# Performance work log

Hardware: AMD Instinct MI355X
Metric: run time of the kernel (lower is better)

## Reference

```python
import jax, jax.numpy as jnp
import numpy as np

B, S, D, H = 64, 256, 2048, 16
HD = D // H  # 128
MAXS = 256


def setup_inputs() -> dict:
    key = jax.random.key(0)
    ks = jax.random.split(key, 16)
    sc = 0.02
    inp = {
        "q": jax.random.normal(ks[0], (B, S, D), jnp.float32),
        "k": jax.random.normal(ks[1], (B, S, D), jnp.float32),
        "v": jax.random.normal(ks[2], (B, S, D), jnp.float32),
        "attention_mask": jax.random.randint(ks[3], (B, S), 0, 2, jnp.int32),
        # projection weights, torch Linear convention: y = x @ W.T + b
        "Wq": jax.random.normal(ks[4], (D, D), jnp.float32) * sc,
        "bq": jnp.zeros((D,), jnp.float32),
        "Wk": jax.random.normal(ks[5], (D, D), jnp.float32) * sc,
        "bk": jnp.zeros((D,), jnp.float32),
        "Wv": jax.random.normal(ks[6], (D, D), jnp.float32) * sc,
        "bv": jnp.zeros((D,), jnp.float32),
        "Wo": jax.random.normal(ks[7], (D, D), jnp.float32) * sc,
        "bo": jnp.zeros((D,), jnp.float32),
        # additive per-head bias table (max_sequence_length=256)
        "bias_table": jax.random.normal(ks[8], (H, MAXS, MAXS), jnp.float32) * 0.1,
    }
    return inp


def reference(q, k, v, attention_mask, Wq, bq, Wk, bk, Wv, bv, Wo, bo, bias_table):
    def proj(x, W, b):  # (B,S,D) -> (B,H,S,HD)
        y = x @ W.T + b
        return y.reshape(B, S, H, HD).transpose(0, 2, 1, 3)

    qh = proj(q, Wq, bq)
    kh = proj(k, Wk, bk)
    vh = proj(v, Wv, bv)

    # (B,H,Sq,Sk) scores
    scores = jnp.einsum("bhqd,bhkd->bhqk", qh, kh) / jnp.sqrt(jnp.float32(HD))
    scores = scores + bias_table[None, :, :S, :S]
    # mask: (B,Sk) -> (B,1,1,Sk); masked_fill where mask==0
    neg_inf = jnp.finfo(scores.dtype).min
    scores = jnp.where(attention_mask[:, None, None, :] == 0, neg_inf, scores)
    probs = jax.nn.softmax(scores, axis=-1)  # dropout p=0.0 -> identity
    out = jnp.einsum("bhqk,bhkd->bhqd", probs, vh)
    out = out.transpose(0, 2, 1, 3).reshape(B, S, D)
    return out @ Wo.T + bo
```

## Files before the change

### kernel.cpp

```cpp
#include <hip/hip_runtime.h>
#include <hip/hip_bf16.h>

typedef __attribute__((ext_vector_type(4))) float f32x4;
typedef __attribute__((ext_vector_type(8))) short s16x8;
typedef __attribute__((ext_vector_type(4))) unsigned short u16x4;
typedef __attribute__((ext_vector_type(8))) unsigned short u16x8;
typedef __attribute__((ext_vector_type(4))) int i32x4;

#define NB 64
#define NS 256
#define ND 2048
#define NH 16
#define NHD 128

__device__ __forceinline__ unsigned short f2bf(float f){
  unsigned int u = __float_as_uint(f);
  u += 0x7fffu + ((u >> 16) & 1u);
  return (unsigned short)(u >> 16);
}

__device__ __forceinline__ void gload16(const void* g, void* l){
  __builtin_amdgcn_global_load_lds(
    (const __attribute__((address_space(1))) unsigned int*)g,
    (__attribute__((address_space(3))) unsigned int*)l, 16, 0, 0);
}

#define SBAR()  __builtin_amdgcn_sched_barrier(0)
#define BARRIER() do{ SBAR(); __builtin_amdgcn_s_barrier(); SBAR(); }while(0)
#define WAIT_LGKM0() do{ asm volatile("s_waitcnt lgkmcnt(0)" ::: "memory"); SBAR(); }while(0)
#define WAIT_VM0()   do{ asm volatile("s_waitcnt vmcnt(0)"   ::: "memory"); SBAR(); }while(0)
#define WAIT_VM4()   do{ asm volatile("s_waitcnt vmcnt(4)"   ::: "memory"); SBAR(); }while(0)

__global__ __launch_bounds__(256) void wconv(const float* __restrict__ s,
                                             unsigned short* __restrict__ d, int n8){
  int i = blockIdx.x*256 + threadIdx.x;
  if (i >= n8) return;
  f32x4 a = *(const f32x4*)(s + (size_t)i*8);
  f32x4 b = *(const f32x4*)(s + (size_t)i*8 + 4);
  u16x8 u;
  #pragma unroll
  for (int r=0;r<4;r++){ u[r]=f2bf(a[r]); u[4+r]=f2bf(b[r]); }
  *(u16x8*)(d + (size_t)i*8) = u;
}

__global__ __launch_bounds__(256) void wconv4(
  const float* __restrict__ s0, const float* __restrict__ s1,
  const float* __restrict__ s2, const float* __restrict__ s3,
  unsigned short* __restrict__ d0, unsigned short* __restrict__ d1,
  unsigned short* __restrict__ d2, unsigned short* __restrict__ d3)
{
  int j = blockIdx.x >> 11;
  const float* s = (j==0)?s0:(j==1)?s1:(j==2)?s2:s3;
  unsigned short* d = (j==0)?d0:(j==1)?d1:(j==2)?d2:d3;
  int i = (blockIdx.x & 2047)*256 + threadIdx.x;
  f32x4 a = *(const f32x4*)(s + (size_t)i*8);
  f32x4 b = *(const f32x4*)(s + (size_t)i*8 + 4);
  u16x8 u;
  #pragma unroll
  for (int r=0;r<4;r++){ u[r]=f2bf(a[r]); u[4+r]=f2bf(b[r]); }
  *(u16x8*)(d + (size_t)i*8) = u;
}

#define GEMM_COMMON_DECLS \
  extern __shared__ __attribute__((aligned(16))) char ldsb[]; \
  const int tid  = threadIdx.x; \
  const int lane = tid & 63, wid = tid >> 6; \
  const int g = lane >> 4, l15 = lane & 15; \
  const int wm = wid >> 2, wn = wid & 3; \
  const int nwg = gridDim.x, bid = blockIdx.x; \
  const int swz = (bid & 7) * (nwg >> 3) + (bid >> 3); \
  const int mt = swz >> 3, nt = swz & 7; \
  const int m0 = mt*256, n0 = nt*256; \
  const int srow_l = tid >> 3, slot = tid & 7;

#define RD_A(buf, qa) do{ \
    _Pragma("unroll") for (int i_=0;i_<4;i_++){ \
      int hr = (qa)*64 + i_*16 + l15; \
      const char* p_ = ldsb + (buf)*65536 + wm*16384 + hr*128; \
      _Pragma("unroll") for (int ks_=0;ks_<2;ks_++) \
        av[i_][ks_] = *(const s16x8*)(p_ + (((ks_*4+g) ^ (hr&7))*16)); } }while(0)

#define RD_B(buf, dst, qb) do{ \
    _Pragma("unroll") for (int j_=0;j_<2;j_++){ \
      int hc = (wn&1)*64 + (qb)*32 + j_*16 + l15; \
      const char* p_ = ldsb + (buf)*65536 + 32768 + (wn>>1)*16384 + hc*128; \
      _Pragma("unroll") for (int ks_=0;ks_<2;ks_++) \
        dst[j_][ks_] = *(const s16x8*)(p_ + (((ks_*4+g) ^ (hc&7))*16)); } }while(0)

#define MFMA_PH(qa, qb, bv) do{ \
    __builtin_amdgcn_s_setprio(1); \
    _Pragma("unroll") for (int i_=0;i_<4;i_++) \
      _Pragma("unroll") for (int j_=0;j_<2;j_++) \
        _Pragma("unroll") for (int ks_=0;ks_<2;ks_++) \
          acc[(qa)*4+i_][(qb)*2+j_] = __builtin_amdgcn_mfma_f32_16x16x32_bf16( \
              av[i_][ks_], bv[j_][ks_], acc[(qa)*4+i_][(qb)*2+j_], 0,0,0); \
    __builtin_amdgcn_s_setprio(0); }while(0)

#define GEMM_EPILOGUE(OUTMODE_) \
  _Pragma("unroll") \
  for (int jx=0;jx<4;jx++){ \
    int n = n0 + wn*64 + ((jx>>1)<<5) + ((jx&1)<<4) + l15; \
    float bj = bias[n]; \
    _Pragma("unroll") \
    for (int i=0;i<8;i++){ \
      int mb = m0 + wm*128 + ((i>>2)<<6) + ((i&3)<<4) + g*4; \
      if ((OUTMODE_) == 2){ \
        float* O = (float*)Out; \
        _Pragma("unroll") for (int r=0;r<4;r++) O[(size_t)(mb+r)*ND + n] = acc[i][jx][r] + bj; \
      } else if ((OUTMODE_) == 0){ \
        unsigned short* O = (unsigned short*)Out; \
        int bb = mb >> 8, h = n >> 7, d = n & 127, s0 = mb & 255; \
        _Pragma("unroll") for (int r=0;r<4;r++) \
          O[(((size_t)bb*NH + h)*NS + s0 + r)*NHD + d] = f2bf(acc[i][jx][r] + bj); \
      } else { \
        unsigned short* O = (unsigned short*)Out; \
        int bb = mb >> 8, h = n >> 7, d = n & 127, s0 = mb & 255; \
        u16x4 u; \
        _Pragma("unroll") for (int r=0;r<4;r++) u[r] = f2bf(acc[i][jx][r] + bj); \
        *(u16x4*)(O + (((size_t)bb*NH + h)*NHD + d)*NS + s0) = u; \
      } \
    } \
  }

template<int OUTMODE>
__global__ __launch_bounds__(512, 2) void gemm256(
    const unsigned short* __restrict__ A, const unsigned short* __restrict__ Bw,
    const float* __restrict__ bias, void* __restrict__ Out)
{
  GEMM_COMMON_DECLS
  const int scol = ((slot ^ (srow_l & 7)) * 8);
  const unsigned short* gsrc[4];
  gsrc[0] = A  + (size_t)(m0 +       srow_l)*ND + scol;
  gsrc[1] = A  + (size_t)(m0 + 128 + srow_l)*ND + scol;
  gsrc[2] = Bw + (size_t)(n0 +       srow_l)*ND + scol;
  gsrc[3] = Bw + (size_t)(n0 + 128 + srow_l)*ND + scol;

#define STAGE(buf, p, kt) do{ \
    const unsigned short* s_ = gsrc[p] + (kt); \
    char* d_ = ldsb + (buf)*65536 + ((p)>>1)*32768 + ((p)&1)*16384 + tid*16; \
    gload16(s_, d_); gload16(s_ + (size_t)64*ND, d_ + 8192); }while(0)

#define HALF(d, ktA, ktB, wmode) do{ \
    RD_A(d,0); RD_B(d,bva,0); \
    if ((ktA)>=0) STAGE((d)^1, 0, ktA); \
    WAIT_LGKM0(); \
    MFMA_PH(0,0,bva); \
    BARRIER(); \
    RD_B(d,bvb,1); \
    if ((ktA)>=0) STAGE((d)^1, 1, ktA); \
    WAIT_LGKM0(); \
    MFMA_PH(0,1,bvb); \
    BARRIER(); \
    RD_A(d,1); \
    if ((ktB)>=0) STAGE(d, 2, ktB); \
    WAIT_LGKM0(); \
    MFMA_PH(1,0,bva); \
    BARRIER(); \
    if ((ktB)>=0) STAGE(d, 3, ktB); \
    MFMA_PH(1,1,bvb); \
    if ((wmode)==0){ WAIT_VM4(); } \
    else if ((wmode)==1){ WAIT_VM0(); } \
    BARRIER(); \
  }while(0)

  f32x4 acc[8][4];
  s16x8 av[4][2], bva[2][2], bvb[2][2];

  STAGE(0,0,0); STAGE(0,1,0); STAGE(0,2,0); STAGE(0,3,0);
  STAGE(1,2,64); STAGE(1,3,64);
  #pragma unroll
  for (int i=0;i<8;i++)
    #pragma unroll
    for (int j=0;j<4;j++) acc[i][j] = f32x4{0.f,0.f,0.f,0.f};
  WAIT_VM4();
  BARRIER();

  for (int t = 0; t < 15; ++t) {
    HALF(0, (2*t+1)*64, (2*t+2)*64, 0);
    HALF(1, (2*t+2)*64, (2*t+3)*64, 0);
  }
  HALF(0, 31*64, -1, 1);
  HALF(1, -1, -1, -1);

  GEMM_EPILOGUE(OUTMODE)
#undef STAGE
#undef HALF
}

__global__ __launch_bounds__(256, 2) void attn_fused5(
  const unsigned short* __restrict__ Qh, const unsigned short* __restrict__ Kh,
  const unsigned short* __restrict__ VT, const int* __restrict__ mask,
  const float* __restrict__ bias_table, unsigned short* __restrict__ AO)
{
  __shared__ unsigned short KV[256*128];
  char* KVb = (char*)KV;
  const int bid = blockIdx.x;
  const int bh = (((bid >> 3) >> 2) << 3) | (bid & 7);
  const int qt = (bid >> 3) & 3;
  const int b = bh >> 4, h = bh & 15;
  const int tid = threadIdx.x, lane = tid & 63, w = tid >> 6;
  const int g = lane >> 4, l15 = lane & 15;
  const int q = qt*64 + w*16 + l15;

  {
    const unsigned short* Ksrc = Kh + (size_t)bh*NS*NHD;
    int r0 = tid >> 4, sl = tid & 15;
    #pragma unroll
    for (int c=0;c<16;c++){
      int row = c*16 + r0;
      gload16(Ksrc + (size_t)row*NHD + ((sl ^ (row&7))*8), KVb + c*4096 + tid*16);
    }
  }
  const unsigned short* Qrow = Qh + ((size_t)bh*NS + q)*NHD;
  s16x8 bq[4];
  #pragma unroll
  for (int kk=0;kk<4;kk++) bq[kk] = *(const s16x8*)(Qrow + kk*32 + g*8);

  WAIT_VM0();
  BARRIER();

  f32x4 c[16];
  __builtin_amdgcn_s_setprio(1);
  #pragma unroll
  for (int kb=0;kb<16;kb++){
    c[kb] = f32x4{0.f,0.f,0.f,0.f};
    int row = kb*16 + l15;
    #pragma unroll
    for (int kk=0;kk<4;kk++){
      s16x8 a = *(const s16x8*)(KVb + row*256 + (((kk*4+g) ^ (row&7))*16));
      c[kb] = __builtin_amdgcn_mfma_f32_16x16x32_bf16(a, bq[kk], c[kb], 0,0,0);
    }
  }
  __builtin_amdgcn_s_setprio(0);

  WAIT_LGKM0();
  BARRIER();

  {
    const unsigned short* Vsrc = VT + (size_t)bh*NHD*NS;
    int r0 = tid >> 5, sl = tid & 31;
    #pragma unroll
    for (int c2=0;c2<16;c2++){
      int row = c2*8 + r0;
      gload16(Vsrc + (size_t)row*NS + ((sl ^ (row&7))*8), KVb + c2*4096 + tid*16);
    }
  }

  const float scale = 0.08838834764831845f;
  const float* brow = bias_table + ((size_t)h*NS + q)*NS;
  const int*   mrow = mask + b*NS;
  float mx = -3.0e38f;
  #pragma unroll
  for (int kb=0;kb<16;kb++){
    f32x4 b4 = *(const f32x4*)(brow + kb*16 + g*4);
    i32x4 m4 = *(const i32x4*)(mrow + kb*16 + g*4);
    #pragma unroll
    for (int r=0;r<4;r++){
      float val = (m4[r] != 0) ? (c[kb][r]*scale + b4[r]) : -3.0e38f;
      c[kb][r] = val;
      mx = fmaxf(mx, val);
    }
  }
  mx = fmaxf(mx, __shfl_xor(mx, 16));
  mx = fmaxf(mx, __shfl_xor(mx, 32));
  float sum = 0.f;
  #pragma unroll
  for (int kb=0;kb<16;kb++)
    #pragma unroll
    for (int r=0;r<4;r++){
      float pv = __expf(c[kb][r] - mx);
      c[kb][r] = pv; sum += pv;
    }
  sum += __shfl_xor(sum, 16);
  sum += __shfl_xor(sum, 32);
  float inv = 1.f / sum;

  unsigned int pk[16][2];
  #pragma unroll
  for (int kb=0;kb<16;kb++){
    pk[kb][0] = (unsigned int)f2bf(c[kb][0]*inv) | ((unsigned int)f2bf(c[kb][1]*inv) << 16);
    pk[kb][1] = (unsigned int)f2bf(c[kb][2]*inv) | ((unsigned int)f2bf(c[kb][3]*inv) << 16);
  }

  WAIT_VM0();
  BARRIER();

  const int s0l = l15 + ((g&1)<<5), s1l = s0l + 16;
  const int sel = g >> 1;
  s16x8 pb[8];
  #pragma unroll
  for (int kk=0;kk<8;kk++){
    unsigned int e0 = (unsigned int)__shfl((int)pk[2*kk][0],   s0l);
    unsigned int e1 = (unsigned int)__shfl((int)pk[2*kk][1],   s0l);
    unsigned int e2 = (unsigned int)__shfl((int)pk[2*kk][0],   s1l);
    unsigned int e3 = (unsigned int)__shfl((int)pk[2*kk][1],   s1l);
    unsigned int o0 = (unsigned int)__shfl((int)pk[2*kk+1][0], s0l);
    unsigned int o1 = (unsigned int)__shfl((int)pk[2*kk+1][1], s0l);
    unsigned int o2 = (unsigned int)__shfl((int)pk[2*kk+1][0], s1l);
    unsigned int o3 = (unsigned int)__shfl((int)pk[2*kk+1][1], s1l);
    union { unsigned int wd[4]; s16x8 v; } u_;
    u_.wd[0] = sel ? o0 : e0; u_.wd[1] = sel ? o1 : e1;
    u_.wd[2] = sel ? o2 : e2; u_.wd[3] = sel ? o3 : e3;
    pb[kk] = u_.v;
  }

  f32x4 oacc[8];
  __builtin_amdgcn_s_setprio(1);
  #pragma unroll
  for (int dt=0;dt<8;dt++){
    oacc[dt] = f32x4{0.f,0.f,0.f,0.f};
    int row = dt*16 + l15;
    #pragma unroll
    for (int kk=0;kk<8;kk++){
      s16x8 a = *(const s16x8*)(KVb + row*512 + (((kk*4+g) ^ (row&7))*16));
      oacc[dt] = __builtin_amdgcn_mfma_f32_16x16x32_bf16(a, pb[kk], oacc[dt], 0,0,0);
    }
  }
  __builtin_amdgcn_s_setprio(0);

  #pragma unroll
  for (int dt=0;dt<8;dt++){
    u16x4 u;
    #pragma unroll
    for (int r=0;r<4;r++) u[r] = f2bf(oacc[dt][r]);
    *(u16x4*)(AO + ((size_t)b*NS + q)*ND + h*NHD + dt*16 + g*4) = u;
  }
}

extern "C" void kernel_launch(void* const* d_in, const int* in_sizes, int n_in,
                              void* d_out, int out_size, void* d_ws, size_t ws_size,
                              hipStream_t stream)
{
  const float* q  = (const float*)d_in[0];
  const float* k  = (const float*)d_in[1];
  const float* v  = (const float*)d_in[2];
  const int* mask = (const int*)d_in[3];
  const float* Wq = (const float*)d_in[4];
  const float* bq = (const float*)d_in[5];
  const float* Wk = (const float*)d_in[6];
  const float* bk = (const float*)d_in[7];
  const float* Wv = (const float*)d_in[8];
  const float* bv = (const float*)d_in[9];
  const float* Wo = (const float*)d_in[10];
  const float* bo = (const float*)d_in[11];
  const float* bias_table = (const float*)d_in[12];

  char* ws = (char*)d_ws;
  unsigned short* Wqb = (unsigned short*)(ws + 0);
  unsigned short* Wkb = (unsigned short*)(ws + 8388608);
  unsigned short* Wvb = (unsigned short*)(ws + 16777216);
  unsigned short* Wob = (unsigned short*)(ws + 25165824);
  unsigned short* tmp = (unsigned short*)(ws + 33554432);
  unsigned short* Qh  = (unsigned short*)(ws + 100663296);
  unsigned short* Kh  = (unsigned short*)(ws + 167772160);
  unsigned short* VT  = (unsigned short*)(ws + 234881024);
  unsigned short* AO  = (unsigned short*)(ws + 301989888);

  hipFuncSetAttribute((const void*)gemm256<0>, hipFuncAttributeMaxDynamicSharedMemorySize, 131072);
  hipFuncSetAttribute((const void*)gemm256<1>, hipFuncAttributeMaxDynamicSharedMemorySize, 131072);
  hipFuncSetAttribute((const void*)gemm256<2>, hipFuncAttributeMaxDynamicSharedMemorySize, 131072);

  wconv4<<<8192,256,0,stream>>>(Wq,Wk,Wv,Wo, Wqb,Wkb,Wvb,Wob);

  const float* acts[3] = {q, k, v};
  const unsigned short* wgt[3] = {Wqb, Wkb, Wvb};
  const float* bia[3] = {bq, bk, bv};
  unsigned short* outs[3] = {Qh, Kh, VT};

  for (int x = 0; x < 3; ++x) {
    wconv<<<16384,256,0,stream>>>(acts[x], tmp, 4194304);
    if (x < 2)
      gemm256<0><<<512,512,131072,stream>>>(tmp, wgt[x], bia[x], outs[x]);
    else
      gemm256<1><<<512,512,131072,stream>>>(tmp, wgt[x], bia[x], outs[x]);
  }

  attn_fused5<<<4096,256,0,stream>>>(Qh,Kh,VT,mask,bias_table,AO);
  gemm256<2><<<512,512,131072,stream>>>(AO,Wob,bo,(float*)d_out);
}
```

Measured before the change: 724.5 us.

## Restage GEMM tiles two steps ahead, drop grid swizzle, prefetch attention bias/mask

The GEMM main loop now refills the buffer it has just finished reading with the tile two steps ahead, as B and then A halves, instead of splitting each tile's loads across both buffers. The vmcnt wait is adjusted to leave that batch of loads in flight. The block-to-tile swizzle is removed, so tiles map directly from the block index, which changes L2 reuse of A and W across concurrent blocks. The attention kernel issues bias-table and mask loads before the QK MFMA loop so their latency overlaps compute, at the cost of about 128 extra VGPRs per thread, which may hurt occupancy.

```diff
diff --git a/kernel.cpp b/kernel.cpp
--- a/kernel.cpp
+++ b/kernel.cpp
@@ -29,7 +29,7 @@
 #define BARRIER() do{ SBAR(); __builtin_amdgcn_s_barrier(); SBAR(); }while(0)
 #define WAIT_LGKM0() do{ asm volatile("s_waitcnt lgkmcnt(0)" ::: "memory"); SBAR(); }while(0)
 #define WAIT_VM0()   do{ asm volatile("s_waitcnt vmcnt(0)"   ::: "memory"); SBAR(); }while(0)
-#define WAIT_VM4()   do{ asm volatile("s_waitcnt vmcnt(4)"   ::: "memory"); SBAR(); }while(0)
+#define WAIT_VM8()   do{ asm volatile("s_waitcnt vmcnt(8)"   ::: "memory"); SBAR(); }while(0)
 
 __global__ __launch_bounds__(256) void wconv(const float* __restrict__ s,
                                              unsigned short* __restrict__ d, int n8){
@@ -67,9 +67,8 @@
   const int lane = tid & 63, wid = tid >> 6; \
   const int g = lane >> 4, l15 = lane & 15; \
   const int wm = wid >> 2, wn = wid & 3; \
-  const int nwg = gridDim.x, bid = blockIdx.x; \
-  const int swz = (bid & 7) * (nwg >> 3) + (bid >> 3); \
-  const int mt = swz >> 3, nt = swz & 7; \
+  const int bid = blockIdx.x; \
+  const int mt = bid >> 3, nt = bid & 7; \
   const int m0 = mt*256, n0 = nt*256; \
   const int srow_l = tid >> 3, slot = tid & 7;
 
@@ -140,25 +139,23 @@
     char* d_ = ldsb + (buf)*65536 + ((p)>>1)*32768 + ((p)&1)*16384 + tid*16; \
     gload16(s_, d_); gload16(s_ + (size_t)64*ND, d_ + 8192); }while(0)
 
-#define HALF(d, ktA, ktB, wmode) do{ \
+#define HALF(d, ktN, wmode) do{ \
     RD_A(d,0); RD_B(d,bva,0); \
-    if ((ktA)>=0) STAGE((d)^1, 0, ktA); \
     WAIT_LGKM0(); \
     MFMA_PH(0,0,bva); \
     BARRIER(); \
     RD_B(d,bvb,1); \
-    if ((ktA)>=0) STAGE((d)^1, 1, ktA); \
     WAIT_LGKM0(); \
     MFMA_PH(0,1,bvb); \
     BARRIER(); \
     RD_A(d,1); \
-    if ((ktB)>=0) STAGE(d, 2, ktB); \
+    if ((ktN)>=0){ STAGE(d,2,ktN); STAGE(d,3,ktN); } \
     WAIT_LGKM0(); \
     MFMA_PH(1,0,bva); \
     BARRIER(); \
-    if ((ktB)>=0) STAGE(d, 3, ktB); \
+    if ((ktN)>=0){ STAGE(d,0,ktN); STAGE(d,1,ktN); } \
     MFMA_PH(1,1,bvb); \
-    if ((wmode)==0){ WAIT_VM4(); } \
+    if ((wmode)==0){ WAIT_VM8(); } \
     else if ((wmode)==1){ WAIT_VM0(); } \
     BARRIER(); \
   }while(0)
@@ -167,27 +164,27 @@
   s16x8 av[4][2], bva[2][2], bvb[2][2];
 
   STAGE(0,0,0); STAGE(0,1,0); STAGE(0,2,0); STAGE(0,3,0);
-  STAGE(1,2,64); STAGE(1,3,64);
+  STAGE(1,0,64); STAGE(1,1,64); STAGE(1,2,64); STAGE(1,3,64);
   #pragma unroll
   for (int i=0;i<8;i++)
     #pragma unroll
     for (int j=0;j<4;j++) acc[i][j] = f32x4{0.f,0.f,0.f,0.f};
-  WAIT_VM4();
+  WAIT_VM8();
   BARRIER();
 
   for (int t = 0; t < 15; ++t) {
-    HALF(0, (2*t+1)*64, (2*t+2)*64, 0);
-    HALF(1, (2*t+2)*64, (2*t+3)*64, 0);
-  }
-  HALF(0, 31*64, -1, 1);
-  HALF(1, -1, -1, -1);
+    HALF(0, (2*t+2)*64, 0);
+    HALF(1, (2*t+3)*64, 0);
+  }
+  HALF(0, -1, 1);
+  HALF(1, -1, -1);
 
   GEMM_EPILOGUE(OUTMODE)
 #undef STAGE
 #undef HALF
 }
 
-__global__ __launch_bounds__(256, 2) void attn_fused5(
+__global__ __launch_bounds__(256, 2) void attn_fused6(
   const unsigned short* __restrict__ Qh, const unsigned short* __restrict__ Kh,
   const unsigned short* __restrict__ VT, const int* __restrict__ mask,
   const float* __restrict__ bias_table, unsigned short* __restrict__ AO)
@@ -215,6 +212,15 @@
   s16x8 bq[4];
   #pragma unroll
   for (int kk=0;kk<4;kk++) bq[kk] = *(const s16x8*)(Qrow + kk*32 + g*8);
+  const float* brow = bias_table + ((size_t)h*NS + q)*NS;
+  const int*   mrow = mask + b*NS;
+  f32x4 br[16];
+  i32x4 mr[16];
+  #pragma unroll
+  for (int kb=0;kb<16;kb++){
+    br[kb] = *(const f32x4*)(brow + kb*16 + g*4);
+    mr[kb] = *(const i32x4*)(mrow + kb*16 + g*4);
+  }
 
   WAIT_VM0();
   BARRIER();
@@ -247,16 +253,12 @@
   }
 
   const float scale = 0.08838834764831845f;
-  const float* brow = bias_table + ((size_t)h*NS + q)*NS;
-  const int*   mrow = mask + b*NS;
   float mx = -3.0e38f;
   #pragma unroll
   for (int kb=0;kb<16;kb++){
-    f32x4 b4 = *(const f32x4*)(brow + kb*16 + g*4);
-    i32x4 m4 = *(const i32x4*)(mrow + kb*16 + g*4);
     #pragma unroll
     for (int r=0;r<4;r++){
-      float val = (m4[r] != 0) ? (c[kb][r]*scale + b4[r]) : -3.0e38f;
+      float val = (mr[kb][r] != 0) ? (c[kb][r]*scale + br[kb][r]) : -3.0e38f;
       c[kb][r] = val;
       mx = fmaxf(mx, val);
     }
@@ -375,6 +377,6 @@
       gemm256<1><<<512,512,131072,stream>>>(tmp, wgt[x], bia[x], outs[x]);
   }
 
-  attn_fused5<<<4096,256,0,stream>>>(Qh,Kh,VT,mask,bias_table,AO);
+  attn_fused6<<<4096,256,0,stream>>>(Qh,Kh,VT,mask,bias_table,AO);
   gemm256<2><<<512,512,131072,stream>>>(AO,Wob,bo,(float*)d_out);
 }
```

Result: slower. 763.2 us (+5.3%).
